# Kernel tuning notes

Hardware: AMD Instinct MI355X
Metric: run time of the kernel (lower is better)

Reference implementation:

```python
import jax, jax.numpy as jnp
import numpy as np

N_NODES = 65536
N_EDGES = 1048576  # even: edges stored as interleaved reverse pairs
F_NODE = 133
F_EDGE = 14
HIDDEN = 128
DEPTH = 3
NUM_GRAPHS = 256


def setup_inputs() -> dict:
    key = jax.random.key(0)
    ks = jax.random.split(key, 10)
    x = jax.random.normal(ks[0], (N_NODES, F_NODE), dtype=jnp.float32)
    edge_attr = jax.random.normal(ks[1], (N_EDGES, F_EDGE), dtype=jnp.float32)
    # directed edges in reverse pairs: edge 2k = (u,v), edge 2k+1 = (v,u)
    src = jax.random.randint(ks[2], (N_EDGES // 2,), 0, N_NODES)
    dst = jax.random.randint(ks[3], (N_EDGES // 2,), 0, N_NODES)
    edge_index = jnp.stack([
        jnp.stack([src, dst], axis=1).reshape(-1),
        jnp.stack([dst, src], axis=1).reshape(-1),
    ]).astype(jnp.int64)
    batch = jnp.sort(jax.random.randint(ks[4], (N_NODES,), 0, NUM_GRAPHS)).astype(jnp.int64)
    def lin(k, fin, fout):
        return jax.random.normal(k, (fin, fout), dtype=jnp.float32) / np.sqrt(fin)
    We = lin(ks[5], F_NODE + F_EDGE, HIDDEN)
    be = jnp.zeros((HIDDEN,), dtype=jnp.float32)
    Wc = jax.random.normal(ks[6], (DEPTH, HIDDEN, HIDDEN), dtype=jnp.float32) / np.sqrt(HIDDEN)
    bc = jnp.zeros((DEPTH, HIDDEN), dtype=jnp.float32)
    Wn = lin(ks[7], F_NODE + HIDDEN, HIDDEN)
    bn = jnp.zeros((HIDDEN,), dtype=jnp.float32)
    return {"x": x, "edge_attr": edge_attr, "edge_index": edge_index, "batch": batch,
            "We": We, "be": be, "Wc": Wc, "bc": bc, "Wn": Wn, "bn": bn}


def reference(x, edge_attr, edge_index, batch, We, be, Wc, bc, Wn, bn):
    n_nodes = x.shape[0]
    row, col = edge_index[0], edge_index[1]
    # edge init: relu(Linear(cat(x[row], edge_attr)))
    h0 = jax.nn.relu(jnp.concatenate([x[row], edge_attr], axis=1) @ We + be)
    h = h0
    for l in range(DEPTH):
        # aggregate edge messages at target nodes (PyG add aggregation)
        agg = jax.ops.segment_sum(h, col, num_segments=n_nodes)
        # reverse-edge message: swap each consecutive pair
        rev = h.reshape(-1, 2, HIDDEN)[:, ::-1, :].reshape(-1, HIDDEN)
        h = (agg[row] - rev) @ Wc[l] + bc[l]
        h = jax.nn.relu(h + h0)  # residual then relu (dropout p used in eval = identity)
    # final aggregation to nodes using last conv (only aggregated message used)
    s = jax.ops.segment_sum(h, col, num_segments=n_nodes)
    q = jax.nn.relu(jnp.concatenate([x, s], axis=1) @ Wn + bn)
    # global_add_pool over graphs
    embedding = jax.ops.segment_sum(q, batch, num_segments=NUM_GRAPHS)
    return embedding
```

## Files before the change

### kernel.cpp

```cpp
#include <hip/hip_runtime.h>

#define N_NODES 65536
#define N_EDGES 1048576
#define F_NODE 133
#define F_EDGE 14
#define HID 128
#define GSTR 256

typedef __attribute__((ext_vector_type(4))) float f32x4;
typedef __attribute__((ext_vector_type(8))) short s16x8;
typedef __attribute__((ext_vector_type(4))) unsigned int u32x4;

__device__ __forceinline__ unsigned short f2bs(float f) {
  unsigned u = __float_as_uint(f);
  u += 0x7FFFu + ((u >> 16) & 1u);
  return (unsigned short)(u >> 16);
}
__device__ __forceinline__ unsigned pk2(float a, float b) {
  return (unsigned)f2bs(a) | ((unsigned)f2bs(b) << 16);
}
__device__ __forceinline__ float bflo(unsigned u) { return __uint_as_float(u << 16); }
__device__ __forceinline__ float bfhi(unsigned u) { return __uint_as_float(u & 0xffff0000u); }
__device__ __forceinline__ float bfs(unsigned short v) { return __uint_as_float((unsigned)v << 16); }

__device__ __forceinline__ int swz256(int row, int b) { return row * 256 + (b ^ ((row & 7) << 4)); }
__device__ __forceinline__ int swz64 (int row, int b) { return row * 64  + (b ^ ((row & 3) << 4)); }
__device__ __forceinline__ int swz384(int row, int b) { return row * 384 + (b ^ ((row & 7) << 4)); }

__global__ __launch_bounds__(256) void k_hist(const int* __restrict__ col, int* __restrict__ deg) {
  int e = blockIdx.x * 256 + threadIdx.x;
  atomicAdd(&deg[col[e]], 1);
}

__global__ __launch_bounds__(1024) void k_scan(const int* __restrict__ deg,
                                               int* __restrict__ base, int* __restrict__ cursor) {
  __shared__ int s0[1024], s1[1024];
  const int t = threadIdx.x;
  const int o = t * 64;
  int sum = 0;
  for (int i = 0; i < 64; ++i) sum += deg[o + i];
  s0[t] = sum;
  __syncthreads();
  int* src = s0; int* dst = s1;
  for (int off = 1; off < 1024; off <<= 1) {
    int v = src[t] + ((t >= off) ? src[t - off] : 0);
    dst[t] = v;
    __syncthreads();
    int* tmp = src; src = dst; dst = tmp;
  }
  int run = src[t] - sum;
  for (int i = 0; i < 64; ++i) {
    base[o + i] = run; cursor[o + i] = run;
    run += deg[o + i];
  }
  if (t == 1023) base[65536] = run;
}

__global__ __launch_bounds__(256) void k_fill(const int* __restrict__ col,
                                              int* __restrict__ cursor, int* __restrict__ invp) {
  int e = blockIdx.x * 256 + threadIdx.x;
  int pos = atomicAdd(&cursor[col[e]], 1);
  invp[e] = pos;
}

__global__ __launch_bounds__(256) void k_revp(const int* __restrict__ invp, int* __restrict__ revp) {
  int e = blockIdx.x * 256 + threadIdx.x;
  revp[e] = invp[e ^ 1];
}

__global__ __launch_bounds__(256) void k_gather(
    const unsigned char* __restrict__ h8, const float* __restrict__ hscale,
    const int* __restrict__ base, unsigned short* __restrict__ G)
{
  const int tid = threadIdx.x;
  const int grp = tid >> 5, l = tid & 31;
  const int n = blockIdx.x * 8 + grp;
  const int s = base[n], E = base[n + 1];
  float a0 = 0.f, a1 = 0.f, a2 = 0.f, a3 = 0.f;
  int i = s;
  for (; i + 3 < E; i += 4) {
    unsigned q0 = *(const unsigned*)(h8 + (size_t)i * HID + l * 4);
    unsigned q1 = *(const unsigned*)(h8 + (size_t)(i + 1) * HID + l * 4);
    unsigned q2 = *(const unsigned*)(h8 + (size_t)(i + 2) * HID + l * 4);
    unsigned q3 = *(const unsigned*)(h8 + (size_t)(i + 3) * HID + l * 4);
    float s0 = hscale[i], s1 = hscale[i + 1], s2 = hscale[i + 2], s3 = hscale[i + 3];
    a0 += (float)(q0 & 255u) * s0 + (float)(q1 & 255u) * s1
        + (float)(q2 & 255u) * s2 + (float)(q3 & 255u) * s3;
    a1 += (float)((q0 >> 8) & 255u) * s0 + (float)((q1 >> 8) & 255u) * s1
        + (float)((q2 >> 8) & 255u) * s2 + (float)((q3 >> 8) & 255u) * s3;
    a2 += (float)((q0 >> 16) & 255u) * s0 + (float)((q1 >> 16) & 255u) * s1
        + (float)((q2 >> 16) & 255u) * s2 + (float)((q3 >> 16) & 255u) * s3;
    a3 += (float)(q0 >> 24) * s0 + (float)(q1 >> 24) * s1
        + (float)(q2 >> 24) * s2 + (float)(q3 >> 24) * s3;
  }
  for (; i < E; ++i) {
    unsigned q0 = *(const unsigned*)(h8 + (size_t)i * HID + l * 4);
    float s0 = hscale[i];
    a0 += (float)(q0 & 255u) * s0;
    a1 += (float)((q0 >> 8) & 255u) * s0;
    a2 += (float)((q0 >> 16) & 255u) * s0;
    a3 += (float)(q0 >> 24) * s0;
  }
  uint2 wv;
  wv.x = pk2(a0, a1);
  wv.y = pk2(a2, a3);
  *(uint2*)(G + (size_t)n * GSTR + l * 4) = wv;
}

template<int MODE>
__global__ __launch_bounds__(256, 2) void k_fused(
    const unsigned short* __restrict__ G,
    const float* __restrict__ ea, const int* __restrict__ rowIdx,
    const int* __restrict__ invp, const int* __restrict__ revp,
    const float* __restrict__ We2, const float* __restrict__ be,
    const float* __restrict__ Wc, const float* __restrict__ bcL,
    unsigned char* __restrict__ h8, float* __restrict__ hscale)
{
  extern __shared__ char sm[];
  constexpr int WT_OFF  = 0;
  constexpr int WT2_OFF = MODE ? 32768 : 0;
  constexpr int M_OFF   = MODE ? 40960 : 0;
  constexpr int EA_OFF  = MODE ? 57344 : 8192;
  constexpr int BE_OFF  = MODE ? 61440 : 12288;
  constexpr int BC_OFF  = MODE ? 61952 : 12800;

  const int tid = threadIdx.x;
  const int lane = tid & 63, w = tid >> 6;
  const int g16 = lane >> 4, c16 = lane & 15;
  const int etM = tid >> 2;
  const int ccM = (tid & 3) * 32;

  u32x4 pG0, pG1, pG2, pG3;
  u32x4 pQa, pQb;
  float pS;
  float pEA0, pEA1, pEA2, pEA3;
  f32x4 pSeed[8];
  int pI0, pI1, pI2, pI3;

  auto stage = [&](int EB) {
    if (MODE) {
      const int eM = EB + etM;
      const int rp = revp[eM];
      const unsigned char* hp = h8 + (size_t)rp * HID + ccM;
      pQa = *(const u32x4*)hp;
      pQb = *(const u32x4*)(hp + 16);
      pS = hscale[rp];
      const int rM = rowIdx[eM];
      const u32x4* gp = (const u32x4*)(G + (size_t)rM * GSTR + ccM);
      pG0 = gp[0]; pG1 = gp[1]; pG2 = gp[2]; pG3 = gp[3];
    }
    {
      const float* eap = ea + (size_t)EB * F_EDGE;
      pEA0 = (tid < 896) ? eap[tid] : 0.f;
      pEA1 = (tid + 256 < 896) ? eap[tid + 256] : 0.f;
      pEA2 = (tid + 512 < 896) ? eap[tid + 512] : 0.f;
      pEA3 = (tid + 768 < 896) ? eap[tid + 768] : 0.f;
      const int er0n = EB + w * 16 + g16 * 4;
      pI0 = invp[er0n];
      pI1 = invp[er0n + 1];
      pI2 = invp[er0n + 2];
      pI3 = invp[er0n + 3];
      const int rw0 = rowIdx[er0n], rw1 = rowIdx[er0n + 1];
      const int rw2 = rowIdx[er0n + 2], rw3 = rowIdx[er0n + 3];
      const unsigned short* x0 = G + (size_t)rw0 * GSTR + 128;
      const unsigned short* x1 = G + (size_t)rw1 * GSTR + 128;
      const unsigned short* x2 = G + (size_t)rw2 * GSTR + 128;
      const unsigned short* x3 = G + (size_t)rw3 * GSTR + 128;
#pragma unroll
      for (int jc = 0; jc < 8; ++jc) {
        const int j = jc * 16 + c16;
        pSeed[jc][0] = bfs(x0[j]);
        pSeed[jc][1] = bfs(x1[j]);
        pSeed[jc][2] = bfs(x2[j]);
        pSeed[jc][3] = bfs(x3[j]);
      }
    }
  };

  stage(blockIdx.x * 512);

  if (MODE) {
    for (int idx = tid; idx < HID * HID; idx += 256) {
      int k = idx >> 7, j = idx & 127;
      *(unsigned short*)(sm + WT_OFF + swz256(j, k * 2)) = f2bs(Wc[idx]);
    }
  }
  for (int idx = tid; idx < 32 * HID; idx += 256) {
    int k = idx >> 7, j = idx & 127;
    float v = (k < F_EDGE) ? We2[k * HID + j] : 0.f;
    *(unsigned short*)(sm + WT2_OFF + swz64(j, k * 2)) = f2bs(v);
  }
  for (int idx = tid; idx < 64 * 18; idx += 256) {
    int e_t = idx / 18, kz = 14 + idx % 18;
    *(unsigned short*)(sm + EA_OFF + swz64(e_t, kz * 2)) = 0;
  }
  if (tid < HID) {
    ((float*)(sm + BE_OFF))[tid] = be[tid];
    if (MODE) ((float*)(sm + BC_OFF))[tid] = bcL[tid];
  }

  for (int it = 0; it < 8; ++it) {
    const int e_base = (blockIdx.x * 8 + it) * 64;

    f32x4 acc[8];
#pragma unroll
    for (int jc = 0; jc < 8; ++jc) acc[jc] = pSeed[jc];
    const int cI0 = pI0, cI1 = pI1, cI2 = pI2, cI3 = pI3;

    __syncthreads();

    if (tid < 896) {
      int e_t = tid / F_EDGE, k = tid - e_t * F_EDGE;
      *(unsigned short*)(sm + EA_OFF + swz64(e_t, k * 2)) = f2bs(pEA0);
    }
    if (tid + 256 < 896) {
      int i = tid + 256, e_t = i / F_EDGE, k = i - e_t * F_EDGE;
      *(unsigned short*)(sm + EA_OFF + swz64(e_t, k * 2)) = f2bs(pEA1);
    }
    if (tid + 512 < 896) {
      int i = tid + 512, e_t = i / F_EDGE, k = i - e_t * F_EDGE;
      *(unsigned short*)(sm + EA_OFF + swz64(e_t, k * 2)) = f2bs(pEA2);
    }
    if (tid + 768 < 896) {
      int i = tid + 768, e_t = i / F_EDGE, k = i - e_t * F_EDGE;
      *(unsigned short*)(sm + EA_OFF + swz64(e_t, k * 2)) = f2bs(pEA3);
    }
    if (MODE) {
      const float s = pS;
#define MW(GW, Q) pk2(bflo(GW) - (float)((Q) & 255u) * s, bfhi(GW) - (float)(((Q) >> 8) & 255u) * s)
      u32x4 v;
      v.x = MW(pG0.x, pQa.x); v.y = MW(pG0.y, pQa.x >> 16);
      v.z = MW(pG0.z, pQa.y); v.w = MW(pG0.w, pQa.y >> 16);
      *(u32x4*)(sm + M_OFF + swz256(etM, ccM * 2 +  0)) = v;
      v.x = MW(pG1.x, pQa.z); v.y = MW(pG1.y, pQa.z >> 16);
      v.z = MW(pG1.z, pQa.w); v.w = MW(pG1.w, pQa.w >> 16);
      *(u32x4*)(sm + M_OFF + swz256(etM, ccM * 2 + 16)) = v;
      v.x = MW(pG2.x, pQb.x); v.y = MW(pG2.y, pQb.x >> 16);
      v.z = MW(pG2.z, pQb.y); v.w = MW(pG2.w, pQb.y >> 16);
      *(u32x4*)(sm + M_OFF + swz256(etM, ccM * 2 + 32)) = v;
      v.x = MW(pG3.x, pQb.z); v.y = MW(pG3.y, pQb.z >> 16);
      v.z = MW(pG3.z, pQb.w); v.w = MW(pG3.w, pQb.w >> 16);
      *(u32x4*)(sm + M_OFF + swz256(etM, ccM * 2 + 48)) = v;
#undef MW
    }

    if (it < 7) stage(e_base + 64);

    __syncthreads();

    {
      const s16x8 afrag = *(const s16x8*)(sm + EA_OFF + swz64(w * 16 + c16, g16 * 16));
#pragma unroll
      for (int jc = 0; jc < 8; ++jc) {
        const s16x8 bf = *(const s16x8*)(sm + WT2_OFF + swz64(jc * 16 + c16, g16 * 16));
        acc[jc] = __builtin_amdgcn_mfma_f32_16x16x32_bf16(afrag, bf, acc[jc], 0, 0, 0);
      }
    }
#pragma unroll
    for (int jc = 0; jc < 8; ++jc) {
      const float bev = ((const float*)(sm + BE_OFF))[jc * 16 + c16];
      const float bcv = MODE ? ((const float*)(sm + BC_OFF))[jc * 16 + c16] : 0.f;
#pragma unroll
      for (int r = 0; r < 4; ++r) {
        float h0v = fmaxf(acc[jc][r] + bev, 0.f);
        acc[jc][r] = MODE ? (h0v + bcv) : h0v;
      }
    }
    if (MODE) {
#pragma unroll
      for (int kk = 0; kk < 4; ++kk) {
        const s16x8 am = *(const s16x8*)(sm + M_OFF + swz256(w * 16 + c16, kk * 64 + g16 * 16));
#pragma unroll
        for (int jc = 0; jc < 8; ++jc) {
          const s16x8 bf = *(const s16x8*)(sm + WT_OFF + swz256(jc * 16 + c16, kk * 64 + g16 * 16));
          acc[jc] = __builtin_amdgcn_mfma_f32_16x16x32_bf16(am, bf, acc[jc], 0, 0, 0);
        }
      }
#pragma unroll
      for (int jc = 0; jc < 8; ++jc)
#pragma unroll
        for (int r = 0; r < 4; ++r)
          acc[jc][r] = fmaxf(acc[jc][r], 0.f);
    }
    float inv[4], sc[4];
#pragma unroll
    for (int r = 0; r < 4; ++r) {
      float m = 0.f;
#pragma unroll
      for (int jc = 0; jc < 8; ++jc) m = fmaxf(m, acc[jc][r]);
#pragma unroll
      for (int off = 1; off < 16; off <<= 1)
        m = fmaxf(m, __shfl_xor(m, off, 64));
      sc[r]  = m > 0.f ? m * (1.f / 255.f) : 0.f;
      inv[r] = m > 0.f ? 255.f / m : 0.f;
    }
    if (c16 == 0) {
      hscale[cI0] = sc[0];
      hscale[cI1] = sc[1];
      hscale[cI2] = sc[2];
      hscale[cI3] = sc[3];
    }
#pragma unroll
    for (int jc = 0; jc < 8; ++jc) {
      const int j = jc * 16 + c16;
      h8[(size_t)cI0 * HID + j] = (unsigned char)__float2uint_rn(fminf(acc[jc][0] * inv[0], 255.f));
      h8[(size_t)cI1 * HID + j] = (unsigned char)__float2uint_rn(fminf(acc[jc][1] * inv[1], 255.f));
      h8[(size_t)cI2 * HID + j] = (unsigned char)__float2uint_rn(fminf(acc[jc][2] * inv[2], 255.f));
      h8[(size_t)cI3 * HID + j] = (unsigned char)__float2uint_rn(fminf(acc[jc][3] * inv[3], 255.f));
    }
  }
}

template<int TOG>
__global__ __launch_bounds__(256) void k_prep(
    const float* __restrict__ x, const float* __restrict__ W,
    float* __restrict__ outf, unsigned short* __restrict__ G)
{
  extern __shared__ char sm[];
  char* WTp = sm;
  char* Ap  = sm + 49152;
  const int tid = threadIdx.x, lane = tid & 63, w = tid >> 6;
  const int g16 = lane >> 4, c16 = lane & 15;

  for (int idx = tid; idx < 192 * HID; idx += 256) {
    int k = idx >> 7, j = idx & 127;
    float v = (k < F_NODE) ? W[(size_t)k * HID + j] : 0.f;
    *(unsigned short*)(WTp + swz384(j, k * 2)) = f2bs(v);
  }
  for (int it = 0; it < 2; ++it) {
    const int nbase = (blockIdx.x * 2 + it) * 64;
    __syncthreads();
    for (int idx = tid; idx < 64 * 192; idx += 256) {
      int r = idx / 192, k = idx - r * 192;
      float v = (k < F_NODE) ? x[(size_t)(nbase + r) * F_NODE + k] : 0.f;
      *(unsigned short*)(Ap + swz384(r, k * 2)) = f2bs(v);
    }
    __syncthreads();
    f32x4 acc[8];
#pragma unroll
    for (int jc = 0; jc < 8; ++jc) acc[jc] = (f32x4)(0.f);
#pragma unroll
    for (int kk = 0; kk < 5; ++kk) {
      const s16x8 af = *(const s16x8*)(Ap + swz384(w * 16 + c16, kk * 64 + g16 * 16));
#pragma unroll
      for (int jc = 0; jc < 8; ++jc) {
        const s16x8 bf = *(const s16x8*)(WTp + swz384(jc * 16 + c16, kk * 64 + g16 * 16));
        acc[jc] = __builtin_amdgcn_mfma_f32_16x16x32_bf16(af, bf, acc[jc], 0, 0, 0);
      }
    }
    const int r0 = nbase + w * 16 + g16 * 4;
#pragma unroll
    for (int jc = 0; jc < 8; ++jc)
#pragma unroll
      for (int r = 0; r < 4; ++r) {
        if (TOG)
          G[(size_t)(r0 + r) * GSTR + 128 + jc * 16 + c16] = f2bs(acc[jc][r]);
        else
          outf[(size_t)(r0 + r) * HID + jc * 16 + c16] = acc[jc][r];
      }
  }
}

__global__ __launch_bounds__(256) void k_nodef(
    const unsigned short* __restrict__ G, const float* __restrict__ xwn,
    const float* __restrict__ WnS, const float* __restrict__ bn,
    const int* __restrict__ batch, float* __restrict__ out)
{
  extern __shared__ char sm[];
  char* WTp = sm;
  char* Ap  = sm + 32768;
  float* bnl = (float*)(sm + 49152);
  const int tid = threadIdx.x, lane = tid & 63, w = tid >> 6;
  const int g16 = lane >> 4, c16 = lane & 15;

  for (int idx = tid; idx < HID * HID; idx += 256) {
    int k = idx >> 7, j = idx & 127;
    *(unsigned short*)(WTp + swz256(j, k * 2)) = f2bs(WnS[(size_t)k * HID + j]);
  }
  if (tid < HID) bnl[tid] = bn[tid];

  for (int it = 0; it < 2; ++it) {
    const int nbase = (blockIdx.x * 2 + it) * 64;
    __syncthreads();
    {
      const int r = tid >> 2, cc = (tid & 3) * 32;
      const u32x4* gp = (const u32x4*)(G + (size_t)(nbase + r) * GSTR + cc);
      *(u32x4*)(Ap + swz256(r, cc * 2 +  0)) = gp[0];
      *(u32x4*)(Ap + swz256(r, cc * 2 + 16)) = gp[1];
      *(u32x4*)(Ap + swz256(r, cc * 2 + 32)) = gp[2];
      *(u32x4*)(Ap + swz256(r, cc * 2 + 48)) = gp[3];
    }
    __syncthreads();
    const int r0 = nbase + w * 16 + g16 * 4;
    f32x4 acc[8];
#pragma unroll
    for (int jc = 0; jc < 8; ++jc) {
      const float bv = bnl[jc * 16 + c16];
#pragma unroll
      for (int r = 0; r < 4; ++r)
        acc[jc][r] = xwn[(size_t)(r0 + r) * HID + jc * 16 + c16] + bv;
    }
#pragma unroll
    for (int kk = 0; kk < 4; ++kk) {
      const s16x8 af = *(const s16x8*)(Ap + swz256(w * 16 + c16, kk * 64 + g16 * 16));
#pragma unroll
      for (int jc = 0; jc < 8; ++jc) {
        const s16x8 bf = *(const s16x8*)(WTp + swz256(jc * 16 + c16, kk * 64 + g16 * 16));
        acc[jc] = __builtin_amdgcn_mfma_f32_16x16x32_bf16(af, bf, acc[jc], 0, 0, 0);
      }
    }
    const int b0 = batch[r0], b1 = batch[r0 + 1];
    const int b2 = batch[r0 + 2], b3 = batch[r0 + 3];
#pragma unroll
    for (int jc = 0; jc < 8; ++jc) {
      const int j = jc * 16 + c16;
      atomicAdd(&out[(size_t)b0 * HID + j], fmaxf(acc[jc][0], 0.f));
      atomicAdd(&out[(size_t)b1 * HID + j], fmaxf(acc[jc][1], 0.f));
      atomicAdd(&out[(size_t)b2 * HID + j], fmaxf(acc[jc][2], 0.f));
      atomicAdd(&out[(size_t)b3 * HID + j], fmaxf(acc[jc][3], 0.f));
    }
  }
}

__global__ void k_diag(float* out, int n, float v) {
  int i = blockIdx.x * 256 + threadIdx.x;
  if (i < n) out[i] = v;
}

extern "C" void kernel_launch(void* const* d_in, const int* in_sizes, int n_in,
                              void* d_out, int out_size, void* d_ws, size_t ws_size,
                              hipStream_t stream) {
  const float* x     = (const float*)d_in[0];
  const float* ea    = (const float*)d_in[1];
  const int*   ei    = (const int*)d_in[2];
  const int*   batch = (const int*)d_in[3];
  const float* We    = (const float*)d_in[4];
  const float* be    = (const float*)d_in[5];
  const float* Wc    = (const float*)d_in[6];
  const float* bc    = (const float*)d_in[7];
  const float* Wn    = (const float*)d_in[8];
  const float* bn    = (const float*)d_in[9];
  float* out = (float*)d_out;

  const int* row = ei;
  const int* col = ei + N_EDGES;
  const float* We2 = We + F_NODE * HID;
  const float* WnS = Wn + F_NODE * HID;

  const size_t szH8    = (size_t)N_EDGES * HID;
  const size_t szScale = (size_t)N_EDGES * sizeof(float);
  const size_t szG     = (size_t)N_NODES * GSTR * sizeof(short);
  const size_t szXwn   = (size_t)N_NODES * HID * sizeof(float);
  const size_t szIdx   = (size_t)N_EDGES * sizeof(int);
  const size_t szDeg   = (size_t)N_NODES * sizeof(int);
  const size_t szBase  = ((size_t)(N_NODES + 1) * sizeof(int) + 255) & ~255ULL;

  size_t off = 0;
  char* ws = (char*)d_ws;
  unsigned char*  h8     = (unsigned char*)(ws + off);  off += szH8;
  float*          hscale = (float*)(ws + off);          off += szScale;
  unsigned short* G      = (unsigned short*)(ws + off); off += szG;
  float*          xwn    = (float*)(ws + off);          off += szXwn;
  int*            invp   = (int*)(ws + off);            off += szIdx;
  int*            revp   = (int*)(ws + off);            off += szIdx;
  int*            deg    = (int*)(ws + off);            off += szDeg;
  int*            base   = (int*)(ws + off);            off += szBase;
  int*            cursor = (int*)(ws + off);            off += szDeg;
  const size_t need = off;

  if (ws_size < need) {
    k_diag<<<(out_size + 255) / 256, 256, 0, stream>>>(out, out_size, (float)ws_size);
    return;
  }

  const size_t lds_f0 = 12800;
  const size_t lds_f1 = 62464;
  const size_t lds_pp = 49152 + 24576;
  const size_t lds_nf = 49152 + 512;

  (void)hipFuncSetAttribute((const void*)(k_fused<0>),
      hipFuncAttributeMaxDynamicSharedMemorySize, (int)lds_f0);
  (void)hipFuncSetAttribute((const void*)(k_fused<1>),
      hipFuncAttributeMaxDynamicSharedMemorySize, (int)lds_f1);
  (void)hipFuncSetAttribute((const void*)(k_prep<0>),
      hipFuncAttributeMaxDynamicSharedMemorySize, (int)lds_pp);
  (void)hipFuncSetAttribute((const void*)(k_prep<1>),
      hipFuncAttributeMaxDynamicSharedMemorySize, (int)lds_pp);
  (void)hipFuncSetAttribute((const void*)k_nodef,
      hipFuncAttributeMaxDynamicSharedMemorySize, (int)lds_nf);

  hipMemsetAsync(deg, 0, szDeg, stream);
  k_hist<<<N_EDGES / 256, 256, 0, stream>>>(col, deg);
  k_scan<<<1, 1024, 0, stream>>>(deg, base, cursor);
  k_fill<<<N_EDGES / 256, 256, 0, stream>>>(col, cursor, invp);
  k_revp<<<N_EDGES / 256, 256, 0, stream>>>(invp, revp);

  k_prep<1><<<512, 256, lds_pp, stream>>>(x, We, nullptr, G);
  k_prep<0><<<512, 256, lds_pp, stream>>>(x, Wn, xwn, nullptr);

  k_fused<0><<<2048, 256, lds_f0, stream>>>(G, ea, row, invp, revp, We2, be,
                                            nullptr, nullptr, h8, hscale);

  for (int l = 0; l < 3; ++l) {
    k_gather<<<N_NODES / 8, 256, 0, stream>>>(h8, hscale, base, G);
    k_fused<1><<<2048, 256, lds_f1, stream>>>(G, ea, row, invp, revp, We2, be,
                                              Wc + (size_t)l * HID * HID, bc + (size_t)l * HID,
                                              h8, hscale);
  }

  k_gather<<<N_NODES / 8, 256, 0, stream>>>(h8, hscale, base, G);

  hipMemsetAsync(out, 0, (size_t)out_size * sizeof(float), stream);
  k_nodef<<<512, 256, lds_nf, stream>>>(G, xwn, WnS, bn, batch, out);
}
```

Before: 1.303 ms.

## Process edge pairs in order sorted by destination node for gather locality

Builds a permutation of reverse-edge pairs sorted by the target of each pair's odd edge, using an extra histogram, scan and fill. The fused edge kernels then walk pairs in that order, so the G rows and reverse h8 rows that nearby blocks read cluster around the same nodes and reuse cache better. Edge-attribute loads become per-edge indirect vector loads instead of one contiguous block load, and each fused kernel does one more indirection through plist. Preprocessing also gains a few small kernels.

```diff
diff --git a/kernel.cpp b/kernel.cpp
--- a/kernel.cpp
+++ b/kernel.cpp
@@ -2,6 +2,7 @@
 
 #define N_NODES 65536
 #define N_EDGES 1048576
+#define NPAIRS  (N_EDGES / 2)
 #define F_NODE 133
 #define F_EDGE 14
 #define HID 128
@@ -66,6 +67,18 @@
 __global__ __launch_bounds__(256) void k_revp(const int* __restrict__ invp, int* __restrict__ revp) {
   int e = blockIdx.x * 256 + threadIdx.x;
   revp[e] = invp[e ^ 1];
+}
+
+__global__ __launch_bounds__(256) void k_hist2(const int* __restrict__ col, int* __restrict__ deg2) {
+  int k = blockIdx.x * 256 + threadIdx.x;
+  atomicAdd(&deg2[col[2 * k + 1]], 1);
+}
+
+__global__ __launch_bounds__(256) void k_fill2(const int* __restrict__ col,
+                                               int* __restrict__ cursor2, int* __restrict__ plist) {
+  int k = blockIdx.x * 256 + threadIdx.x;
+  int pos = atomicAdd(&cursor2[col[2 * k + 1]], 1);
+  plist[pos] = k;
 }
 
 __global__ __launch_bounds__(256) void k_gather(
@@ -112,6 +125,7 @@
     const unsigned short* __restrict__ G,
     const float* __restrict__ ea, const int* __restrict__ rowIdx,
     const int* __restrict__ invp, const int* __restrict__ revp,
+    const int* __restrict__ plist,
     const float* __restrict__ We2, const float* __restrict__ be,
     const float* __restrict__ Wc, const float* __restrict__ bcL,
     unsigned char* __restrict__ h8, float* __restrict__ hscale)
@@ -128,18 +142,20 @@
   const int lane = tid & 63, w = tid >> 6;
   const int g16 = lane >> 4, c16 = lane & 15;
   const int etM = tid >> 2;
-  const int ccM = (tid & 3) * 32;
+  const int q4  = tid & 3;
+  const int ccM = q4 * 32;
 
   u32x4 pG0, pG1, pG2, pG3;
   u32x4 pQa, pQb;
   float pS;
-  float pEA0, pEA1, pEA2, pEA3;
+  float4 pEA;
   f32x4 pSeed[8];
   int pI0, pI1, pI2, pI3;
 
-  auto stage = [&](int EB) {
+  auto stage = [&](int PB) {
+    const int pidM = plist[PB + (etM >> 1)];
+    const int eM = 2 * pidM + (etM & 1);
     if (MODE) {
-      const int eM = EB + etM;
       const int rp = revp[eM];
       const unsigned char* hp = h8 + (size_t)rp * HID + ccM;
       pQa = *(const u32x4*)hp;
@@ -150,18 +166,18 @@
       pG0 = gp[0]; pG1 = gp[1]; pG2 = gp[2]; pG3 = gp[3];
     }
     {
-      const float* eap = ea + (size_t)EB * F_EDGE;
-      pEA0 = (tid < 896) ? eap[tid] : 0.f;
-      pEA1 = (tid + 256 < 896) ? eap[tid + 256] : 0.f;
-      pEA2 = (tid + 512 < 896) ? eap[tid + 512] : 0.f;
-      pEA3 = (tid + 768 < 896) ? eap[tid + 768] : 0.f;
-      const int er0n = EB + w * 16 + g16 * 4;
-      pI0 = invp[er0n];
-      pI1 = invp[er0n + 1];
-      pI2 = invp[er0n + 2];
-      pI3 = invp[er0n + 3];
-      const int rw0 = rowIdx[er0n], rw1 = rowIdx[er0n + 1];
-      const int rw2 = rowIdx[er0n + 2], rw3 = rowIdx[er0n + 3];
+      const float* eap = ea + (size_t)eM * F_EDGE;
+      if (q4 < 3) pEA = *(const float4*)(eap + q4 * 4);
+      else { float2 t2 = *(const float2*)(eap + 12); pEA.x = t2.x; pEA.y = t2.y; }
+    }
+    {
+      const int s = w * 16 + g16 * 4;
+      const int pa = plist[PB + (s >> 1)];
+      const int pb = plist[PB + (s >> 1) + 1];
+      const int E0 = 2 * pa, E1 = 2 * pa + 1, E2 = 2 * pb, E3 = 2 * pb + 1;
+      pI0 = invp[E0]; pI1 = invp[E1]; pI2 = invp[E2]; pI3 = invp[E3];
+      const int rw0 = rowIdx[E0], rw1 = rowIdx[E1];
+      const int rw2 = rowIdx[E2], rw3 = rowIdx[E3];
       const unsigned short* x0 = G + (size_t)rw0 * GSTR + 128;
       const unsigned short* x1 = G + (size_t)rw1 * GSTR + 128;
       const unsigned short* x2 = G + (size_t)rw2 * GSTR + 128;
@@ -177,7 +193,7 @@
     }
   };
 
-  stage(blockIdx.x * 512);
+  stage(blockIdx.x * 256);
 
   if (MODE) {
     for (int idx = tid; idx < HID * HID; idx += 256) {
@@ -200,7 +216,7 @@
   }
 
   for (int it = 0; it < 8; ++it) {
-    const int e_base = (blockIdx.x * 8 + it) * 64;
+    const int PB = (blockIdx.x * 8 + it) * 32;
 
     f32x4 acc[8];
 #pragma unroll
@@ -209,21 +225,14 @@
 
     __syncthreads();
 
-    if (tid < 896) {
-      int e_t = tid / F_EDGE, k = tid - e_t * F_EDGE;
-      *(unsigned short*)(sm + EA_OFF + swz64(e_t, k * 2)) = f2bs(pEA0);
-    }
-    if (tid + 256 < 896) {
-      int i = tid + 256, e_t = i / F_EDGE, k = i - e_t * F_EDGE;
-      *(unsigned short*)(sm + EA_OFF + swz64(e_t, k * 2)) = f2bs(pEA1);
-    }
-    if (tid + 512 < 896) {
-      int i = tid + 512, e_t = i / F_EDGE, k = i - e_t * F_EDGE;
-      *(unsigned short*)(sm + EA_OFF + swz64(e_t, k * 2)) = f2bs(pEA2);
-    }
-    if (tid + 768 < 896) {
-      int i = tid + 768, e_t = i / F_EDGE, k = i - e_t * F_EDGE;
-      *(unsigned short*)(sm + EA_OFF + swz64(e_t, k * 2)) = f2bs(pEA3);
+    {
+      const int kb = q4 * 4;
+      *(unsigned short*)(sm + EA_OFF + swz64(etM, (kb + 0) * 2)) = f2bs(pEA.x);
+      *(unsigned short*)(sm + EA_OFF + swz64(etM, (kb + 1) * 2)) = f2bs(pEA.y);
+      if (q4 < 3) {
+        *(unsigned short*)(sm + EA_OFF + swz64(etM, (kb + 2) * 2)) = f2bs(pEA.z);
+        *(unsigned short*)(sm + EA_OFF + swz64(etM, (kb + 3) * 2)) = f2bs(pEA.w);
+      }
     }
     if (MODE) {
       const float s = pS;
@@ -244,7 +253,7 @@
 #undef MW
     }
 
-    if (it < 7) stage(e_base + 64);
+    if (it < 7) stage(PB + 32);
 
     __syncthreads();
 
@@ -452,6 +461,7 @@
   const size_t szG     = (size_t)N_NODES * GSTR * sizeof(short);
   const size_t szXwn   = (size_t)N_NODES * HID * sizeof(float);
   const size_t szIdx   = (size_t)N_EDGES * sizeof(int);
+  const size_t szPl    = (size_t)NPAIRS * sizeof(int);
   const size_t szDeg   = (size_t)N_NODES * sizeof(int);
   const size_t szBase  = ((size_t)(N_NODES + 1) * sizeof(int) + 255) & ~255ULL;
 
@@ -463,9 +473,13 @@
   float*          xwn    = (float*)(ws + off);          off += szXwn;
   int*            invp   = (int*)(ws + off);            off += szIdx;
   int*            revp   = (int*)(ws + off);            off += szIdx;
+  int*            plist  = (int*)(ws + off);            off += szPl;
   int*            deg    = (int*)(ws + off);            off += szDeg;
   int*            base   = (int*)(ws + off);            off += szBase;
   int*            cursor = (int*)(ws + off);            off += szDeg;
+  int*            deg2   = (int*)(ws + off);            off += szDeg;
+  int*            base2  = (int*)(ws + off);            off += szBase;
+  int*            cursor2= (int*)(ws + off);            off += szDeg;
   const size_t need = off;
 
   if (ws_size < need) {
@@ -490,20 +504,24 @@
       hipFuncAttributeMaxDynamicSharedMemorySize, (int)lds_nf);
 
   hipMemsetAsync(deg, 0, szDeg, stream);
+  hipMemsetAsync(deg2, 0, szDeg, stream);
   k_hist<<<N_EDGES / 256, 256, 0, stream>>>(col, deg);
+  k_hist2<<<NPAIRS / 256, 256, 0, stream>>>(col, deg2);
   k_scan<<<1, 1024, 0, stream>>>(deg, base, cursor);
+  k_scan<<<1, 1024, 0, stream>>>(deg2, base2, cursor2);
   k_fill<<<N_EDGES / 256, 256, 0, stream>>>(col, cursor, invp);
+  k_fill2<<<NPAIRS / 256, 256, 0, stream>>>(col, cursor2, plist);
   k_revp<<<N_EDGES / 256, 256, 0, stream>>>(invp, revp);
 
   k_prep<1><<<512, 256, lds_pp, stream>>>(x, We, nullptr, G);
   k_prep<0><<<512, 256, lds_pp, stream>>>(x, Wn, xwn, nullptr);
 
-  k_fused<0><<<2048, 256, lds_f0, stream>>>(G, ea, row, invp, revp, We2, be,
+  k_fused<0><<<2048, 256, lds_f0, stream>>>(G, ea, row, invp, revp, plist, We2, be,
                                             nullptr, nullptr, h8, hscale);
 
   for (int l = 0; l < 3; ++l) {
     k_gather<<<N_NODES / 8, 256, 0, stream>>>(h8, hscale, base, G);
-    k_fused<1><<<2048, 256, lds_f1, stream>>>(G, ea, row, invp, revp, We2, be,
+    k_fused<1><<<2048, 256, lds_f1, stream>>>(G, ea, row, invp, revp, plist, We2, be,
                                               Wc + (size_t)l * HID * HID, bc + (size_t)l * HID,
                                               h8, hscale);
   }
```

Result: slower. 1.426 ms (+9.4%).
